# Performance work log

Measured on AMD Instinct MI355X. Metric: run time of the kernel, lower is better.

Reference implementation:

```python
import jax, jax.numpy as jnp
import numpy as np

D_DYN, D_STAT, H, T, B = 3, 3, 256, 365, 1024


def setup_inputs() -> dict:
    key = jax.random.key(0)
    ks = jax.random.split(key, 8)
    C = D_DYN + H
    s = lambda k, shape: jax.random.normal(k, shape, dtype=jnp.float32) * 0.05
    return {
        "x_dyn": jax.random.normal(ks[0], (B, T, D_DYN), dtype=jnp.float32),
        "x_stat": jax.random.normal(ks[1], (B, D_STAT), dtype=jnp.float32),
        "w_i": s(ks[2], (D_STAT, H)), "b_i": jnp.zeros((H,), jnp.float32),
        "w_f": s(ks[3], (C, H)), "b_f": jnp.zeros((H,), jnp.float32),
        "w_g": s(ks[4], (C, H)), "b_g": jnp.zeros((H,), jnp.float32),
        "w_o": s(ks[5], (C, H)), "b_o": jnp.zeros((H,), jnp.float32),
        "w_head": s(ks[6], (H, 1)), "b_head": jnp.zeros((1,), jnp.float32),
    }


def reference(x_dyn, x_stat, w_i, b_i, w_f, b_f, w_g, b_g, w_o, b_o, w_head, b_head):
    # Static input gate (EA-LSTM): i depends only on static features.
    i = jax.nn.sigmoid(x_stat @ w_i + b_i)  # (B, H)

    # Merge the three gate linears into one (C, 3H) matmul per step and
    # split the concat [x_t, h] into x- and h-parts (equivalent to torch.cat).
    W = jnp.concatenate([w_f, w_g, w_o], axis=1)  # (C, 3H)
    Wx, Wh = W[:D_DYN], W[D_DYN:]                 # (D,3H), (H,3H)
    b = jnp.concatenate([b_f, b_g, b_o])          # (3H,)

    def step(carry, x_t):
        h, c = carry
        z = x_t @ Wx + h @ Wh + b                 # (B, 3H)
        f = jax.nn.sigmoid(z[:, :H])
        g = jnp.tanh(z[:, H:2 * H])
        o = jax.nn.sigmoid(z[:, 2 * H:])
        c = f * c + i * g
        h = o * jnp.tanh(c)
        return (h, c), None

    h0 = jnp.zeros((x_dyn.shape[0], H), x_dyn.dtype)
    c0 = jnp.zeros((x_dyn.shape[0], H), x_dyn.dtype)
    (h, _), _ = jax.lax.scan(step, (h0, c0), jnp.swapaxes(x_dyn, 0, 1))
    # Dropout is identity in eval mode.
    return h @ w_head + b_head  # (B, 1)
```

## Files before the change

kernel.cpp:

```cpp
#include <hip/hip_runtime.h>
#include <hip/hip_bf16.h>

#define T_STEPS 365
#define XLEN    (T_STEPS * 3)
#define H_SZ    256
#define ROWS    4
#define NBLK    256
#define NW      8
#define CPW     32

#define SF1     (-1.4426950408889634f)
#define SF2     (-2.8853900817779268f)

typedef __attribute__((ext_vector_type(8))) short bf16x8;
typedef __attribute__((ext_vector_type(4))) short bf16x4;
typedef __attribute__((ext_vector_type(4))) float f32x4;

__device__ __forceinline__ float fast_sigmoid(float x) {
    return __builtin_amdgcn_rcpf(1.0f + __builtin_amdgcn_exp2f(-1.44269504f * x));
}
__device__ __forceinline__ unsigned short f2bf(float x) {
    __hip_bfloat16 b = __float2bfloat16(x);
    return *reinterpret_cast<unsigned short*>(&b);
}
__device__ __forceinline__ float bf2f(unsigned short v) {
    return __uint_as_float(((unsigned)v) << 16);
}

__global__ void __launch_bounds__(512, 2)
ealstm_fused(const float* __restrict__ x_dyn, const float* __restrict__ x_stat,
             const float* __restrict__ w_i, const float* __restrict__ b_i,
             const float* __restrict__ w_f, const float* __restrict__ b_f,
             const float* __restrict__ w_g, const float* __restrict__ b_g,
             const float* __restrict__ w_o, const float* __restrict__ b_o,
             const float* __restrict__ w_head, const float* __restrict__ b_head,
             float* __restrict__ out)
{
    const int tid   = threadIdx.x;
    const int lane  = tid & 63;
    const int wv    = tid >> 6;
    const int m     = lane & 15;
    const int l16   = lane >> 4;
    const int rb    = blockIdx.x * ROWS;
    const int wbase = wv * CPW;

    const int r_eff  = m & 3;
    const int ct_eff = m >> 3;
    const int qp     = ((m >> 2) & 1) * 2;

    __shared__ unsigned short wo_lds[4 * 8 * 256 * 8];
    __shared__ unsigned short hbuf[2][4096];
    __shared__ float          red[NW][ROWS];

    for (int idx = tid; idx < 4 * 8 * 8 * 256; idx += 512) {
        const int c    = idx & 255;
        const int e    = (idx >> 8) & 7;
        const int kt   = (idx >> 11) & 7;
        const int l16g = idx >> 14;
        wo_lds[((l16g * 8 + kt) * 256 + c) * 8 + e] =
            f2bf(SF1 * w_o[(3 + kt * 32 + l16g * 8 + e) * H_SZ + c]);
    }
    for (int idx = tid; idx < 4096; idx += 512) ((unsigned int*)hbuf)[idx] = 0u;

    const float* wsrc[3] = {w_f, w_g, w_o};
    const float* bsrc[3] = {b_f, b_g, b_o};
    const float  gsf[3]  = {SF1, SF2, SF1};

    bf16x8 wA[8][2][2];
#pragma unroll
    for (int ct = 0; ct < 2; ++ct) {
        const int c = wbase + ct * 16 + m;
#pragma unroll
        for (int g = 0; g < 2; ++g)
#pragma unroll
            for (int kt = 0; kt < 8; ++kt) {
                bf16x8 a;
#pragma unroll
                for (int e = 0; e < 8; ++e)
                    a[e] = (short)f2bf(gsf[g] * wsrc[g][(3 + kt * 32 + l16 * 8 + e) * H_SZ + c]);
                wA[kt][ct][g] = a;
            }
    }

    const int cw0 = wbase + ct_eff * 16 + l16 * 4 + qp;
    f32x4 cxw[2][3];
#pragma unroll
    for (int e = 0; e < 2; ++e)
#pragma unroll
        for (int g = 0; g < 3; ++g) {
            const int c = cw0 + e;
            f32x4 v;
            v[0] = gsf[g] * wsrc[g][0 * H_SZ + c];
            v[1] = gsf[g] * wsrc[g][1 * H_SZ + c];
            v[2] = gsf[g] * wsrc[g][2 * H_SZ + c];
            v[3] = gsf[g] * bsrc[g][c];
            cxw[e][g] = v;
        }

    float iv[2], cst[2];
    {
        const float xs0 = x_stat[(rb + r_eff) * 3 + 0];
        const float xs1 = x_stat[(rb + r_eff) * 3 + 1];
        const float xs2 = x_stat[(rb + r_eff) * 3 + 2];
#pragma unroll
        for (int e = 0; e < 2; ++e) {
            const int c = cw0 + e;
            iv[e] = fast_sigmoid(b_i[c] + xs0 * w_i[c] + xs1 * w_i[H_SZ + c]
                                        + xs2 * w_i[2 * H_SZ + c]);
            cst[e] = 0.0f;
        }
    }

    const int kw  = cw0 >> 5;
    const int kp  = cw0 & 31;
    const int woff = ((kw * 64) + r_eff + 16 * (kp >> 3)) * 8 + (kp & 7);

    const float*  xr     = x_dyn + (size_t)(rb + r_eff) * XLEN;
    const bf16x8* wobase = (const bf16x8*)&wo_lds[((l16 * 8) * 256 + wbase + m) * 8];

    __syncthreads();

    for (int t = 0; t < T_STEPS; ++t) {
        const int cur = t & 1;
        const bf16x8* hp = (const bf16x8*)hbuf[cur] + lane;
        unsigned short* hw = hbuf[cur ^ 1];

        const float x0 = xr[t * 3 + 0];
        const float x1 = xr[t * 3 + 1];
        const float x2 = xr[t * 3 + 2];

        f32x4 acc[2][3];
        {
            const f32x4 z4 = {0.f, 0.f, 0.f, 0.f};
            const bf16x8 b0  = hp[0];
            const bf16x8 wo0 = wobase[0];
            const bf16x8 wo1 = wobase[16];
            acc[0][0] = __builtin_amdgcn_mfma_f32_16x16x32_bf16(wA[0][0][0], b0, z4, 0, 0, 0);
            acc[0][1] = __builtin_amdgcn_mfma_f32_16x16x32_bf16(wA[0][0][1], b0, z4, 0, 0, 0);
            acc[0][2] = __builtin_amdgcn_mfma_f32_16x16x32_bf16(wo0,         b0, z4, 0, 0, 0);
            acc[1][0] = __builtin_amdgcn_mfma_f32_16x16x32_bf16(wA[0][1][0], b0, z4, 0, 0, 0);
            acc[1][1] = __builtin_amdgcn_mfma_f32_16x16x32_bf16(wA[0][1][1], b0, z4, 0, 0, 0);
            acc[1][2] = __builtin_amdgcn_mfma_f32_16x16x32_bf16(wo1,         b0, z4, 0, 0, 0);
        }
#pragma unroll
        for (int kt = 1; kt < 8; ++kt) {
            const bf16x8 b   = hp[kt * 64];
            const bf16x8 wo0 = wobase[kt * 256];
            const bf16x8 wo1 = wobase[kt * 256 + 16];
            acc[0][0] = __builtin_amdgcn_mfma_f32_16x16x32_bf16(wA[kt][0][0], b, acc[0][0], 0, 0, 0);
            acc[0][1] = __builtin_amdgcn_mfma_f32_16x16x32_bf16(wA[kt][0][1], b, acc[0][1], 0, 0, 0);
            acc[0][2] = __builtin_amdgcn_mfma_f32_16x16x32_bf16(wo0,          b, acc[0][2], 0, 0, 0);
            acc[1][0] = __builtin_amdgcn_mfma_f32_16x16x32_bf16(wA[kt][1][0], b, acc[1][0], 0, 0, 0);
            acc[1][1] = __builtin_amdgcn_mfma_f32_16x16x32_bf16(wA[kt][1][1], b, acc[1][1], 0, 0, 0);
            acc[1][2] = __builtin_amdgcn_mfma_f32_16x16x32_bf16(wo1,          b, acc[1][2], 0, 0, 0);
        }

        float zA[3][4];
#pragma unroll
        for (int q = 0; q < 4; ++q) {
#pragma unroll
            for (int g = 0; g < 3; ++g) {
                const float s = __shfl_xor(acc[1][g][q], 8);
                zA[g][q] = (m >= 8) ? s : acc[0][g][q];
            }
        }
        float z[3][2];
#pragma unroll
        for (int g = 0; g < 3; ++g) {
            const float u2 = __shfl_xor(zA[g][2], 4);
            const float u3 = __shfl_xor(zA[g][3], 4);
            z[g][0] = (m & 4) ? u2 : zA[g][0];
            z[g][1] = (m & 4) ? u3 : zA[g][1];
        }

        unsigned short h2[2];
#pragma unroll
        for (int e = 0; e < 2; ++e) {
            const float zf = z[0][e] + cxw[e][0][3] + x0 * cxw[e][0][0] + x1 * cxw[e][0][1] + x2 * cxw[e][0][2];
            const float zg = z[1][e] + cxw[e][1][3] + x0 * cxw[e][1][0] + x1 * cxw[e][1][1] + x2 * cxw[e][1][2];
            const float zo = z[2][e] + cxw[e][2][3] + x0 * cxw[e][2][0] + x1 * cxw[e][2][1] + x2 * cxw[e][2][2];
            const float Ef = __builtin_amdgcn_exp2f(zf);
            const float Eg = __builtin_amdgcn_exp2f(zg);
            const float Eo = __builtin_amdgcn_exp2f(zo);
            const float u  = 1.0f + Eg;
            const float v  = 1.0f + Ef;
            const float t2 = iv[e] * (2.0f - u);
            const float cq = (cst[e] * u + t2 * v) * __builtin_amdgcn_rcpf(u * v);
            cst[e] = cq;
            const float Ec = __builtin_amdgcn_exp2f(SF2 * cq);
            const float hq = (1.0f - Ec) * __builtin_amdgcn_rcpf((1.0f + Eo) * (1.0f + Ec));
            h2[e] = f2bf(hq);
        }
        {
            unsigned int pk = (unsigned)h2[0] | ((unsigned)h2[1] << 16);
            *(unsigned int*)&hw[woff] = pk;
        }
        __syncthreads();
    }

    float p = 0.0f;
    {
        const unsigned short* hf = hbuf[1];
        const unsigned int hv = *(const unsigned int*)&hf[woff];
        p = bf2f((unsigned short)(hv & 0xffff)) * w_head[cw0]
          + bf2f((unsigned short)(hv >> 16))    * w_head[cw0 + 1];
    }
    p += __shfl_xor(p, 4);
    p += __shfl_xor(p, 8);
    p += __shfl_xor(p, 16);
    p += __shfl_xor(p, 32);
    if (lane < ROWS) red[wv][lane] = p;
    __syncthreads();
    if (tid < ROWS) {
        float s = b_head[0];
#pragma unroll
        for (int w = 0; w < NW; ++w) s += red[w][tid];
        out[rb + tid] = s;
    }
}

extern "C" void kernel_launch(void* const* d_in, const int* in_sizes, int n_in,
                              void* d_out, int out_size, void* d_ws, size_t ws_size,
                              hipStream_t stream)
{
    const float* x_dyn  = (const float*)d_in[0];
    const float* x_stat = (const float*)d_in[1];
    const float* w_i    = (const float*)d_in[2];
    const float* b_i    = (const float*)d_in[3];
    const float* w_f    = (const float*)d_in[4];
    const float* b_f    = (const float*)d_in[5];
    const float* w_g    = (const float*)d_in[6];
    const float* b_g    = (const float*)d_in[7];
    const float* w_o    = (const float*)d_in[8];
    const float* b_o    = (const float*)d_in[9];
    const float* w_head = (const float*)d_in[10];
    const float* b_head = (const float*)d_in[11];

    ealstm_fused<<<dim3(NBLK), dim3(512), 0, stream>>>(
        x_dyn, x_stat, w_i, b_i, w_f, b_f, w_g, b_g, w_o, b_o,
        w_head, b_head, (float*)d_out);
}
```

Measured before the change: 524.3 us.

## Halve waves per block, give each wave 64 hidden columns with mostly register-resident weights

Each block now uses 4 waves instead of 8, and each wave computes 64 hidden columns. The f and g weights and six of the eight k-tiles of the o weights are held in registers; only the last two o k-tiles stay in LDS. Input-projection coefficients move to an LDS table, and each lane now writes four h values per step. The goal is to cut the cost of the per-step barrier and the LDS weight traffic, at the price of very high register pressure (one block per CU) and fewer waves to hide latency.

```diff
diff --git a/kernel.cpp b/kernel.cpp
--- a/kernel.cpp
+++ b/kernel.cpp
@@ -6,8 +6,8 @@
 #define H_SZ    256
 #define ROWS    4
 #define NBLK    256
-#define NW      8
-#define CPW     32
+#define NW      4
+#define CPW     64
 
 #define SF1     (-1.4426950408889634f)
 #define SF2     (-2.8853900817779268f)
@@ -27,7 +27,7 @@
     return __uint_as_float(((unsigned)v) << 16);
 }
 
-__global__ void __launch_bounds__(512, 2)
+__global__ void __launch_bounds__(256, 1)
 ealstm_fused(const float* __restrict__ x_dyn, const float* __restrict__ x_stat,
              const float* __restrict__ w_i, const float* __restrict__ b_i,
              const float* __restrict__ w_f, const float* __restrict__ b_f,
@@ -45,30 +45,46 @@
     const int wbase = wv * CPW;
 
     const int r_eff  = m & 3;
-    const int ct_eff = m >> 3;
-    const int qp     = ((m >> 2) & 1) * 2;
-
-    __shared__ unsigned short wo_lds[4 * 8 * 256 * 8];
+    const int ct_eff = ((m >> 3) << 1) | ((m >> 2) & 1);
+
+    __shared__ unsigned short wo_lds[4 * 2 * 256 * 8];
     __shared__ unsigned short hbuf[2][4096];
+    __shared__ f32x4          cof4[12 * 256];
     __shared__ float          red[NW][ROWS];
-
-    for (int idx = tid; idx < 4 * 8 * 8 * 256; idx += 512) {
-        const int c    = idx & 255;
-        const int e    = (idx >> 8) & 7;
-        const int kt   = (idx >> 11) & 7;
-        const int l16g = idx >> 14;
-        wo_lds[((l16g * 8 + kt) * 256 + c) * 8 + e] =
-            f2bf(SF1 * w_o[(3 + kt * 32 + l16g * 8 + e) * H_SZ + c]);
-    }
-    for (int idx = tid; idx < 4096; idx += 512) ((unsigned int*)hbuf)[idx] = 0u;
 
     const float* wsrc[3] = {w_f, w_g, w_o};
     const float* bsrc[3] = {b_f, b_g, b_o};
     const float  gsf[3]  = {SF1, SF2, SF1};
 
-    bf16x8 wA[8][2][2];
-#pragma unroll
-    for (int ct = 0; ct < 2; ++ct) {
+    for (int idx = tid; idx < 4 * 2 * 8 * 256; idx += 256) {
+        const int c    = idx & 255;
+        const int e    = (idx >> 8) & 7;
+        const int kt2  = (idx >> 11) & 1;
+        const int l16g = idx >> 12;
+        wo_lds[((l16g * 2 + kt2) * 256 + c) * 8 + e] =
+            f2bf(SF1 * w_o[(3 + (kt2 + 6) * 32 + l16g * 8 + e) * H_SZ + c]);
+    }
+    {
+        const int cw0 = wbase + ct_eff * 16 + l16 * 4;
+#pragma unroll
+        for (int g = 0; g < 3; ++g)
+#pragma unroll
+            for (int q = 0; q < 4; ++q) {
+                const int c = cw0 + q;
+                f32x4 v;
+                v[0] = gsf[g] * wsrc[g][0 * H_SZ + c];
+                v[1] = gsf[g] * wsrc[g][1 * H_SZ + c];
+                v[2] = gsf[g] * wsrc[g][2 * H_SZ + c];
+                v[3] = gsf[g] * bsrc[g][c];
+                cof4[(g * 4 + q) * 256 + tid] = v;
+            }
+    }
+    for (int idx = tid; idx < 4096; idx += 256) ((unsigned int*)hbuf)[idx] = 0u;
+
+    bf16x8 wFG[8][4][2];
+    bf16x8 wO[6][4];
+#pragma unroll
+    for (int ct = 0; ct < 4; ++ct) {
         const int c = wbase + ct * 16 + m;
 #pragma unroll
         for (int g = 0; g < 2; ++g)
@@ -78,45 +94,37 @@
 #pragma unroll
                 for (int e = 0; e < 8; ++e)
                     a[e] = (short)f2bf(gsf[g] * wsrc[g][(3 + kt * 32 + l16 * 8 + e) * H_SZ + c]);
-                wA[kt][ct][g] = a;
-            }
-    }
-
-    const int cw0 = wbase + ct_eff * 16 + l16 * 4 + qp;
-    f32x4 cxw[2][3];
-#pragma unroll
-    for (int e = 0; e < 2; ++e)
-#pragma unroll
-        for (int g = 0; g < 3; ++g) {
-            const int c = cw0 + e;
-            f32x4 v;
-            v[0] = gsf[g] * wsrc[g][0 * H_SZ + c];
-            v[1] = gsf[g] * wsrc[g][1 * H_SZ + c];
-            v[2] = gsf[g] * wsrc[g][2 * H_SZ + c];
-            v[3] = gsf[g] * bsrc[g][c];
-            cxw[e][g] = v;
-        }
-
-    float iv[2], cst[2];
+                wFG[kt][ct][g] = a;
+            }
+#pragma unroll
+        for (int kt = 0; kt < 6; ++kt) {
+            bf16x8 a;
+#pragma unroll
+            for (int e = 0; e < 8; ++e)
+                a[e] = (short)f2bf(SF1 * w_o[(3 + kt * 32 + l16 * 8 + e) * H_SZ + c]);
+            wO[kt][ct] = a;
+        }
+    }
+
+    const int cw0 = wbase + ct_eff * 16 + l16 * 4;
+    float iv[4], cst[4];
     {
         const float xs0 = x_stat[(rb + r_eff) * 3 + 0];
         const float xs1 = x_stat[(rb + r_eff) * 3 + 1];
         const float xs2 = x_stat[(rb + r_eff) * 3 + 2];
 #pragma unroll
-        for (int e = 0; e < 2; ++e) {
-            const int c = cw0 + e;
-            iv[e] = fast_sigmoid(b_i[c] + xs0 * w_i[c] + xs1 * w_i[H_SZ + c]
+        for (int q = 0; q < 4; ++q) {
+            const int c = cw0 + q;
+            iv[q] = fast_sigmoid(b_i[c] + xs0 * w_i[c] + xs1 * w_i[H_SZ + c]
                                         + xs2 * w_i[2 * H_SZ + c]);
-            cst[e] = 0.0f;
-        }
-    }
-
-    const int kw  = cw0 >> 5;
-    const int kp  = cw0 & 31;
-    const int woff = ((kw * 64) + r_eff + 16 * (kp >> 3)) * 8 + (kp & 7);
+            cst[q] = 0.0f;
+        }
+    }
+
+    const int woff = ((cw0 >> 5) * 64 + r_eff + 16 * ((cw0 & 31) >> 3)) * 8 + (cw0 & 7);
 
     const float*  xr     = x_dyn + (size_t)(rb + r_eff) * XLEN;
-    const bf16x8* wobase = (const bf16x8*)&wo_lds[((l16 * 8) * 256 + wbase + m) * 8];
+    const bf16x8* wobase = (const bf16x8*)wo_lds;
 
     __syncthreads();
 
@@ -129,81 +137,89 @@
         const float x1 = xr[t * 3 + 1];
         const float x2 = xr[t * 3 + 2];
 
-        f32x4 acc[2][3];
+        bf16x8 wot[2][4];
+#pragma unroll
+        for (int k2 = 0; k2 < 2; ++k2)
+#pragma unroll
+            for (int ct = 0; ct < 4; ++ct)
+                wot[k2][ct] = wobase[(l16 * 2 + k2) * 256 + wbase + ct * 16 + m];
+
+        f32x4 acc[4][3];
         {
             const f32x4 z4 = {0.f, 0.f, 0.f, 0.f};
-            const bf16x8 b0  = hp[0];
-            const bf16x8 wo0 = wobase[0];
-            const bf16x8 wo1 = wobase[16];
-            acc[0][0] = __builtin_amdgcn_mfma_f32_16x16x32_bf16(wA[0][0][0], b0, z4, 0, 0, 0);
-            acc[0][1] = __builtin_amdgcn_mfma_f32_16x16x32_bf16(wA[0][0][1], b0, z4, 0, 0, 0);
-            acc[0][2] = __builtin_amdgcn_mfma_f32_16x16x32_bf16(wo0,         b0, z4, 0, 0, 0);
-            acc[1][0] = __builtin_amdgcn_mfma_f32_16x16x32_bf16(wA[0][1][0], b0, z4, 0, 0, 0);
-            acc[1][1] = __builtin_amdgcn_mfma_f32_16x16x32_bf16(wA[0][1][1], b0, z4, 0, 0, 0);
-            acc[1][2] = __builtin_amdgcn_mfma_f32_16x16x32_bf16(wo1,         b0, z4, 0, 0, 0);
+            const bf16x8 b0 = hp[0];
+#pragma unroll
+            for (int ct = 0; ct < 4; ++ct) {
+                acc[ct][0] = __builtin_amdgcn_mfma_f32_16x16x32_bf16(wFG[0][ct][0], b0, z4, 0, 0, 0);
+                acc[ct][1] = __builtin_amdgcn_mfma_f32_16x16x32_bf16(wFG[0][ct][1], b0, z4, 0, 0, 0);
+                acc[ct][2] = __builtin_amdgcn_mfma_f32_16x16x32_bf16(wO[0][ct],     b0, z4, 0, 0, 0);
+            }
         }
 #pragma unroll
         for (int kt = 1; kt < 8; ++kt) {
-            const bf16x8 b   = hp[kt * 64];
-            const bf16x8 wo0 = wobase[kt * 256];
-            const bf16x8 wo1 = wobase[kt * 256 + 16];
-            acc[0][0] = __builtin_amdgcn_mfma_f32_16x16x32_bf16(wA[kt][0][0], b, acc[0][0], 0, 0, 0);
-            acc[0][1] = __builtin_amdgcn_mfma_f32_16x16x32_bf16(wA[kt][0][1], b, acc[0][1], 0, 0, 0);
-            acc[0][2] = __builtin_amdgcn_mfma_f32_16x16x32_bf16(wo0,          b, acc[0][2], 0, 0, 0);
-            acc[1][0] = __builtin_amdgcn_mfma_f32_16x16x32_bf16(wA[kt][1][0], b, acc[1][0], 0, 0, 0);
-            acc[1][1] = __builtin_amdgcn_mfma_f32_16x16x32_bf16(wA[kt][1][1], b, acc[1][1], 0, 0, 0);
-            acc[1][2] = __builtin_amdgcn_mfma_f32_16x16x32_bf16(wo1,          b, acc[1][2], 0, 0, 0);
-        }
-
-        float zA[3][4];
+            const bf16x8 b = hp[kt * 64];
+#pragma unroll
+            for (int ct = 0; ct < 4; ++ct) {
+                const bf16x8 wo = (kt < 6) ? wO[kt][ct] : wot[kt - 6][ct];
+                acc[ct][0] = __builtin_amdgcn_mfma_f32_16x16x32_bf16(wFG[kt][ct][0], b, acc[ct][0], 0, 0, 0);
+                acc[ct][1] = __builtin_amdgcn_mfma_f32_16x16x32_bf16(wFG[kt][ct][1], b, acc[ct][1], 0, 0, 0);
+                acc[ct][2] = __builtin_amdgcn_mfma_f32_16x16x32_bf16(wo,             b, acc[ct][2], 0, 0, 0);
+            }
+        }
+
+        float accQ[2][3][4];
+#pragma unroll
+        for (int j = 0; j < 2; ++j)
+#pragma unroll
+            for (int g = 0; g < 3; ++g)
+#pragma unroll
+                for (int q = 0; q < 4; ++q) {
+                    const float s = __shfl_xor(acc[2 * j + 1][g][q], 4);
+                    accQ[j][g][q] = (m & 4) ? s : acc[2 * j][g][q];
+                }
+        float z[3][4];
+#pragma unroll
+        for (int g = 0; g < 3; ++g)
+#pragma unroll
+            for (int q = 0; q < 4; ++q) {
+                const float s = __shfl_xor(accQ[1][g][q], 8);
+                z[g][q] = (m & 8) ? s : accQ[0][g][q];
+            }
+
+#pragma unroll
+        for (int g = 0; g < 3; ++g)
+#pragma unroll
+            for (int q = 0; q < 4; ++q) {
+                const f32x4 w = cof4[(g * 4 + q) * 256 + tid];
+                z[g][q] += w[3] + x0 * w[0] + x1 * w[1] + x2 * w[2];
+            }
+
+        bf16x4 pk;
 #pragma unroll
         for (int q = 0; q < 4; ++q) {
-#pragma unroll
-            for (int g = 0; g < 3; ++g) {
-                const float s = __shfl_xor(acc[1][g][q], 8);
-                zA[g][q] = (m >= 8) ? s : acc[0][g][q];
-            }
-        }
-        float z[3][2];
-#pragma unroll
-        for (int g = 0; g < 3; ++g) {
-            const float u2 = __shfl_xor(zA[g][2], 4);
-            const float u3 = __shfl_xor(zA[g][3], 4);
-            z[g][0] = (m & 4) ? u2 : zA[g][0];
-            z[g][1] = (m & 4) ? u3 : zA[g][1];
-        }
-
-        unsigned short h2[2];
-#pragma unroll
-        for (int e = 0; e < 2; ++e) {
-            const float zf = z[0][e] + cxw[e][0][3] + x0 * cxw[e][0][0] + x1 * cxw[e][0][1] + x2 * cxw[e][0][2];
-            const float zg = z[1][e] + cxw[e][1][3] + x0 * cxw[e][1][0] + x1 * cxw[e][1][1] + x2 * cxw[e][1][2];
-            const float zo = z[2][e] + cxw[e][2][3] + x0 * cxw[e][2][0] + x1 * cxw[e][2][1] + x2 * cxw[e][2][2];
-            const float Ef = __builtin_amdgcn_exp2f(zf);
-            const float Eg = __builtin_amdgcn_exp2f(zg);
-            const float Eo = __builtin_amdgcn_exp2f(zo);
+            const float Ef = __builtin_amdgcn_exp2f(z[0][q]);
+            const float Eg = __builtin_amdgcn_exp2f(z[1][q]);
+            const float Eo = __builtin_amdgcn_exp2f(z[2][q]);
             const float u  = 1.0f + Eg;
             const float v  = 1.0f + Ef;
-            const float t2 = iv[e] * (2.0f - u);
-            const float cq = (cst[e] * u + t2 * v) * __builtin_amdgcn_rcpf(u * v);
-            cst[e] = cq;
+            const float t2 = iv[q] * (2.0f - u);
+            const float cq = (cst[q] * u + t2 * v) * __builtin_amdgcn_rcpf(u * v);
+            cst[q] = cq;
             const float Ec = __builtin_amdgcn_exp2f(SF2 * cq);
             const float hq = (1.0f - Ec) * __builtin_amdgcn_rcpf((1.0f + Eo) * (1.0f + Ec));
-            h2[e] = f2bf(hq);
-        }
-        {
-            unsigned int pk = (unsigned)h2[0] | ((unsigned)h2[1] << 16);
-            *(unsigned int*)&hw[woff] = pk;
-        }
+            pk[q] = (short)f2bf(hq);
+        }
+        *(bf16x4*)&hw[woff] = pk;
         __syncthreads();
     }
 
     float p = 0.0f;
     {
         const unsigned short* hf = hbuf[1];
-        const unsigned int hv = *(const unsigned int*)&hf[woff];
-        p = bf2f((unsigned short)(hv & 0xffff)) * w_head[cw0]
-          + bf2f((unsigned short)(hv >> 16))    * w_head[cw0 + 1];
+        const f32x4 wh = *(const f32x4*)&w_head[cw0];
+        const bf16x4 hv = *(const bf16x4*)&hf[woff];
+#pragma unroll
+        for (int q = 0; q < 4; ++q) p += bf2f((unsigned short)hv[q]) * wh[q];
     }
     p += __shfl_xor(p, 4);
     p += __shfl_xor(p, 8);
@@ -236,7 +252,7 @@
     const float* w_head = (const float*)d_in[10];
     const float* b_head = (const float*)d_in[11];
 
-    ealstm_fused<<<dim3(NBLK), dim3(512), 0, stream>>>(
+    ealstm_fused<<<dim3(NBLK), dim3(256), 0, stream>>>(
         x_dyn, x_stat, w_i, b_i, w_f, b_f, w_g, b_g, w_o, b_o,
         w_head, b_head, (float*)d_out);
 }
```

Result: slower. 910.5 us (+73.7%).
